# Kernel optimization log

Measured on AMD Instinct MI355X. Metric: run time of the kernel, lower is better.

## Reference

```python
import jax, jax.numpy as jnp
import numpy as np

B, S, DEC, ENC = 64, 4096, 512, 256


def setup_inputs() -> dict:
    key = jax.random.key(0)
    ks = jax.random.split(key, 8)
    scale_d = 1.0 / np.sqrt(DEC)
    scale_e = 1.0 / np.sqrt(ENC)
    return {
        "decoder_hidden": jax.random.normal(ks[0], (B, 1, DEC), jnp.float32),
        "encoder_outputs": jax.random.normal(ks[1], (B, S, ENC), jnp.float32),
        "mask": jax.random.randint(ks[2], (B, S), 0, 2, jnp.int32),
        "Wd": jax.random.normal(ks[3], (DEC, ENC), jnp.float32) * scale_d,
        "bd": jnp.zeros((ENC,), jnp.float32),
        "We": jax.random.normal(ks[4], (ENC, ENC), jnp.float32) * scale_e,
        "be": jnp.zeros((ENC,), jnp.float32),
        "Wa": jax.random.normal(ks[5], (ENC,), jnp.float32) * scale_e,
        "ba": jnp.zeros((1,), jnp.float32),
    }


def reference(decoder_hidden, encoder_outputs, mask, Wd, bd, We, be, Wa, ba):
    # decoder_proj: [B,1,ENC]; encoder_proj: [B,S,ENC]
    decoder_proj = jnp.einsum("bqd,de->bqe", decoder_hidden, Wd) + bd
    encoder_proj = jnp.einsum("bse,ef->bsf", encoder_outputs, We) + be
    energy = jnp.tanh(decoder_proj + encoder_proj)          # [B,S,ENC]
    scores = jnp.einsum("bse,e->bs", energy, Wa) + ba[0]     # [B,S]
    scores = jnp.where(mask == 0, jnp.float32(-1e10), scores)
    attn = jax.nn.softmax(scores, axis=1)                    # [B,S]
    context = jnp.einsum("bs,bse->be", attn, encoder_outputs)[:, None, :]  # [B,1,ENC]
    return context, attn
```

## Files before the change

kernel.cpp:

```cpp
#include <hip/hip_runtime.h>

#define BATCH 64
#define SEQ   4096
#define DECD  512
#define ENC   256
#define TS    128
#define NCHUNK (SEQ / TS)
#define OUT_ATTN (BATCH * ENC)

typedef short  short8  __attribute__((ext_vector_type(8)));
typedef float  floatx4 __attribute__((ext_vector_type(4)));

__device__ __forceinline__ short f2bf(float f) {
    union { float f; unsigned u; } v; v.f = f;
    unsigned u = v.u;
    u += 0x7FFFu + ((u >> 16) & 1u);
    return (short)(u >> 16);
}

__device__ __forceinline__ float fast_tanh(float x) {
    x = fminf(fmaxf(x, -9.0f), 9.0f);
    float e2 = __expf(2.0f * x);
    float r  = __builtin_amdgcn_rcpf(e2 + 1.0f);
    return fmaf(-2.0f, r, 1.0f);
}

__device__ __forceinline__ void gload_lds16(const short* g, short* l) {
    __builtin_amdgcn_global_load_lds(
        (const __attribute__((address_space(1))) unsigned int*)g,
        (__attribute__((address_space(3))) unsigned int*)l,
        16, 0, 0);
}

__global__ void dp_kernel(const float* __restrict__ dh,
                          const float* __restrict__ Wd,
                          const float* __restrict__ bd,
                          const float* __restrict__ be,
                          float* __restrict__ dpb4) {
    __shared__ float dhs[128];
    int blk = blockIdx.x, b = blk >> 2, j = blk & 3;
    int t = threadIdx.x;
    if (t < 128) dhs[t] = dh[b * DECD + j * 128 + t];
    __syncthreads();
    const float* wp = Wd + (size_t)(j * 128) * ENC + t;
    float a0 = 0.f, a1 = 0.f, a2 = 0.f, a3 = 0.f;
#pragma unroll 4
    for (int d = 0; d < 128; d += 4) {
        a0 = fmaf(dhs[d],     wp[(size_t)(d)     * ENC], a0);
        a1 = fmaf(dhs[d + 1], wp[(size_t)(d + 1) * ENC], a1);
        a2 = fmaf(dhs[d + 2], wp[(size_t)(d + 2) * ENC], a2);
        a3 = fmaf(dhs[d + 3], wp[(size_t)(d + 3) * ENC], a3);
    }
    float r = (a0 + a1) + (a2 + a3);
    if (j == 0) r += bd[t] + be[t];
    dpb4[(size_t)(b * 4 + j) * ENC + t] = r;
}

__global__ void pack_kernel(const float* __restrict__ We, short* __restrict__ WeF) {
    int gid  = blockIdx.x * 256 + threadIdx.x;
    int lane = gid & 63;
    int nt   = (gid >> 6) & 15;
    int kt   = gid >> 10;
    int quad = lane >> 4, l16 = lane & 15;
    int n = nt * 16 + l16;
    short8 v;
#pragma unroll
    for (int j = 0; j < 8; ++j) {
        int k = kt * 32 + quad * 8 + j;
        v[j] = f2bf(We[k * ENC + n]);
    }
    *(short8*)(WeF + gid * 8) = v;
}

__global__ __launch_bounds__(512, 4) void main_kernel(
    const float* __restrict__ enc, const int* __restrict__ mask,
    const short* __restrict__ WeF, const float* __restrict__ dpb4,
    const float* __restrict__ Wa, const float* __restrict__ ba,
    float* __restrict__ out, float* __restrict__ ctx_ws, float* __restrict__ ml_ws)
{
    __shared__ short Bs[32768];
    float* F    = (float*)Bs;
    float* scF  = F;
    float* wgtF = F + 128;
    float* dpbF = F + 256;
    float* waF  = F + 512;

    int blk   = blockIdx.x;
    int b     = blk >> 5;
    int chunk = blk & 31;
    int s_base = chunk * TS;
    int t    = threadIdx.x;
    int w    = t >> 6, lane = t & 63;
    int quad = lane >> 4, l16 = lane & 15;

    const float* encB = enc + (size_t)b * SEQ * ENC;
    int row = s_base + w * 16 + l16;
    const float* aRow = encB + (size_t)row * ENC + quad * 8;

    floatx4 acc[16];
#pragma unroll
    for (int nt = 0; nt < 16; ++nt) acc[nt] = (floatx4){0.f, 0.f, 0.f, 0.f};

    floatx4 p0[3], p1[3];
#pragma unroll
    for (int p = 0; p < 3; ++p) {
        p0[p] = *(const floatx4*)(aRow + p * 32);
        p1[p] = *(const floatx4*)(aRow + p * 32 + 4);
    }

#pragma unroll
    for (int j = 0; j < 8; ++j) {
        int c = j * 8 + w;
        gload_lds16(WeF + c * 512 + lane * 8, Bs + c * 512 + lane * 8);
    }
    __syncthreads();

#pragma unroll
    for (int kkt = 0; kkt < 4; ++kkt) {
        const int s = kkt % 3;
        short8 a;
#pragma unroll
        for (int j = 0; j < 4; ++j) { a[j] = f2bf(p0[s][j]); a[j + 4] = f2bf(p1[s][j]); }
        if (kkt < 5) {
            p0[s] = *(const floatx4*)(aRow + (kkt + 3) * 32);
            p1[s] = *(const floatx4*)(aRow + (kkt + 3) * 32 + 4);
        }
        const short* bp = Bs + kkt * 8192 + lane * 8;
#pragma unroll
        for (int ng = 0; ng < 4; ++ng) {
            short8 bf0 = *(const short8*)(bp + (ng * 4 + 0) * 512);
            short8 bf1 = *(const short8*)(bp + (ng * 4 + 1) * 512);
            short8 bf2 = *(const short8*)(bp + (ng * 4 + 2) * 512);
            short8 bf3 = *(const short8*)(bp + (ng * 4 + 3) * 512);
            acc[ng * 4 + 0] = __builtin_amdgcn_mfma_f32_16x16x32_bf16(a, bf0, acc[ng * 4 + 0], 0, 0, 0);
            acc[ng * 4 + 1] = __builtin_amdgcn_mfma_f32_16x16x32_bf16(a, bf1, acc[ng * 4 + 1], 0, 0, 0);
            acc[ng * 4 + 2] = __builtin_amdgcn_mfma_f32_16x16x32_bf16(a, bf2, acc[ng * 4 + 2], 0, 0, 0);
            acc[ng * 4 + 3] = __builtin_amdgcn_mfma_f32_16x16x32_bf16(a, bf3, acc[ng * 4 + 3], 0, 0, 0);
        }
    }

    __syncthreads();
#pragma unroll
    for (int j = 0; j < 8; ++j) {
        int c = j * 8 + w;
        gload_lds16(WeF + 32768 + c * 512 + lane * 8, Bs + c * 512 + lane * 8);
    }
    __syncthreads();

#pragma unroll
    for (int kkt = 4; kkt < 8; ++kkt) {
        const int s = kkt % 3;
        short8 a;
#pragma unroll
        for (int j = 0; j < 4; ++j) { a[j] = f2bf(p0[s][j]); a[j + 4] = f2bf(p1[s][j]); }
        if (kkt < 5) {
            p0[s] = *(const floatx4*)(aRow + (kkt + 3) * 32);
            p1[s] = *(const floatx4*)(aRow + (kkt + 3) * 32 + 4);
        }
        const short* bp = Bs + (kkt - 4) * 8192 + lane * 8;
#pragma unroll
        for (int ng = 0; ng < 4; ++ng) {
            short8 bf0 = *(const short8*)(bp + (ng * 4 + 0) * 512);
            short8 bf1 = *(const short8*)(bp + (ng * 4 + 1) * 512);
            short8 bf2 = *(const short8*)(bp + (ng * 4 + 2) * 512);
            short8 bf3 = *(const short8*)(bp + (ng * 4 + 3) * 512);
            acc[ng * 4 + 0] = __builtin_amdgcn_mfma_f32_16x16x32_bf16(a, bf0, acc[ng * 4 + 0], 0, 0, 0);
            acc[ng * 4 + 1] = __builtin_amdgcn_mfma_f32_16x16x32_bf16(a, bf1, acc[ng * 4 + 1], 0, 0, 0);
            acc[ng * 4 + 2] = __builtin_amdgcn_mfma_f32_16x16x32_bf16(a, bf2, acc[ng * 4 + 2], 0, 0, 0);
            acc[ng * 4 + 3] = __builtin_amdgcn_mfma_f32_16x16x32_bf16(a, bf3, acc[ng * 4 + 3], 0, 0, 0);
        }
    }

    __syncthreads();
    if (t < 256) {
        const float* dp = dpb4 + (size_t)b * 4 * ENC;
        dpbF[t] = dp[t] + dp[ENC + t] + dp[2 * ENC + t] + dp[3 * ENC + t];
    } else {
        waF[t - 256] = Wa[t - 256];
    }
    __syncthreads();

    float ba0 = ba[0];
    float part[4] = {0.f, 0.f, 0.f, 0.f};
#pragma unroll
    for (int nt = 0; nt < 16; ++nt) {
        int n = nt * 16 + l16;
        float wa  = waF[n];
        float dpv = dpbF[n];
#pragma unroll
        for (int r = 0; r < 4; ++r)
            part[r] = fmaf(wa, fast_tanh(acc[nt][r] + dpv), part[r]);
    }
#pragma unroll
    for (int r = 0; r < 4; ++r) {
        float v = part[r];
        v += __shfl_xor(v, 1);
        v += __shfl_xor(v, 2);
        v += __shfl_xor(v, 4);
        v += __shfl_xor(v, 8);
        part[r] = v;
    }
    if (l16 == 0) {
        int idx0 = w * 16 + quad * 4;
        int s0 = s_base + idx0;
        const int4 mv = *(const int4*)(mask + b * SEQ + s0);
        int mvals[4] = {mv.x, mv.y, mv.z, mv.w};
#pragma unroll
        for (int r = 0; r < 4; ++r) {
            float scv = part[r] + ba0;
            if (mvals[r] == 0) scv = -1e10f;
            scF[idx0 + r] = scv;
            out[OUT_ATTN + (size_t)b * SEQ + s0 + r] = scv;
        }
    }
    __syncthreads();

    float v0 = scF[lane], v1 = scF[lane + 64];
    float m = fmaxf(v0, v1);
    m = fmaxf(m, __shfl_xor(m, 1));
    m = fmaxf(m, __shfl_xor(m, 2));
    m = fmaxf(m, __shfl_xor(m, 4));
    m = fmaxf(m, __shfl_xor(m, 8));
    m = fmaxf(m, __shfl_xor(m, 16));
    m = fmaxf(m, __shfl_xor(m, 32));
    float e0 = __expf(v0 - m), e1 = __expf(v1 - m);
    float l = e0 + e1;
    l += __shfl_xor(l, 1);
    l += __shfl_xor(l, 2);
    l += __shfl_xor(l, 4);
    l += __shfl_xor(l, 8);
    l += __shfl_xor(l, 16);
    l += __shfl_xor(l, 32);
    if (t < TS) wgtF[t] = __expf(scF[t] - m);
    __syncthreads();

    int ecol = t & 255, seg = t >> 8;
    float c0 = 0.f, c1 = 0.f, c2 = 0.f, c3 = 0.f;
    const float* ep = encB + (size_t)(s_base + seg * 64) * ENC + ecol;
    const float* wp = wgtF + seg * 64;
#pragma unroll 4
    for (int s2 = 0; s2 < 64; s2 += 4) {
        c0 = fmaf(wp[s2],     ep[(size_t)(s2)     * ENC], c0);
        c1 = fmaf(wp[s2 + 1], ep[(size_t)(s2 + 1) * ENC], c1);
        c2 = fmaf(wp[s2 + 2], ep[(size_t)(s2 + 2) * ENC], c2);
        c3 = fmaf(wp[s2 + 3], ep[(size_t)(s2 + 3) * ENC], c3);
    }
    float ctx = (c0 + c1) + (c2 + c3);

    int cidx = b * NCHUNK + chunk;
    ctx_ws[((size_t)cidx * 2 + seg) * ENC + ecol] = ctx;
    if (t == 0) {
        ml_ws[cidx * 2]     = m;
        ml_ws[cidx * 2 + 1] = l;
    }
}

__global__ void final_kernel(const float* __restrict__ ctx_ws,
                             const float* __restrict__ ml_ws,
                             float* __restrict__ out) {
    int b = blockIdx.x, t = threadIdx.x;
    float m = -3.4e38f;
    for (int c = 0; c < NCHUNK; ++c)
        m = fmaxf(m, ml_ws[(b * NCHUNK + c) * 2]);
    float L = 0.f;
    for (int c = 0; c < NCHUNK; ++c)
        L += ml_ws[(b * NCHUNK + c) * 2 + 1] * __expf(ml_ws[(b * NCHUNK + c) * 2] - m);
    float inv = 1.0f / L;

    float cx = 0.f;
    for (int c = 0; c < NCHUNK; ++c) {
        float sc_c = __expf(ml_ws[(b * NCHUNK + c) * 2] - m);
        size_t base = ((size_t)(b * NCHUNK + c) * 2) * ENC + t;
        cx += sc_c * (ctx_ws[base] + ctx_ws[base + ENC]);
    }
    out[b * ENC + t] = cx * inv;

    for (int s = t; s < SEQ; s += 256) {
        float raw = out[OUT_ATTN + (size_t)b * SEQ + s];
        out[OUT_ATTN + (size_t)b * SEQ + s] = __expf(raw - m) * inv;
    }
}

extern "C" void kernel_launch(void* const* d_in, const int* in_sizes, int n_in,
                              void* d_out, int out_size, void* d_ws, size_t ws_size,
                              hipStream_t stream) {
    const float* dh   = (const float*)d_in[0];
    const float* enc  = (const float*)d_in[1];
    const int*   mask = (const int*)d_in[2];
    const float* Wd   = (const float*)d_in[3];
    const float* bd   = (const float*)d_in[4];
    const float* We   = (const float*)d_in[5];
    const float* be   = (const float*)d_in[6];
    const float* Wa   = (const float*)d_in[7];
    const float* ba   = (const float*)d_in[8];
    float* out = (float*)d_out;

    float* w      = (float*)d_ws;
    float* ctx_ws = w;
    float* ml_ws  = w + BATCH * NCHUNK * 2 * ENC;
    float* dpb4   = ml_ws + BATCH * NCHUNK * 2;
    short* WeF    = (short*)(dpb4 + BATCH * 4 * ENC);

    hipLaunchKernelGGL(dp_kernel,   dim3(BATCH * 4),       dim3(256), 0, stream, dh, Wd, bd, be, dpb4);
    hipLaunchKernelGGL(pack_kernel, dim3(32),              dim3(256), 0, stream, We, WeF);
    hipLaunchKernelGGL(main_kernel, dim3(BATCH * NCHUNK),  dim3(512), 0, stream,
                       enc, mask, WeF, dpb4, Wa, ba, out, ctx_ws, ml_ws);
    hipLaunchKernelGGL(final_kernel, dim3(BATCH),          dim3(256), 0, stream, ctx_ws, ml_ws, out);
}
```

Measured before the change: 416.5 us.

## Reuse register-held bf16 encoder tiles for context, merge prep kernels, widen final grid

The main kernel now loads and converts the whole encoder row slice to bf16 registers up front. The context sum reuses those register values through shuffle reductions and LDS instead of re-reading the encoder tile from global memory. The dp and pack kernels are merged into one launch, and the final kernel is spread over 8 blocks per batch so the attention normalisation runs with more parallelism. In exchange, the context is now computed from bf16-rounded encoder values, which costs precision, and more registers are held live, which may lower occupancy.

After: 491.7 us. +18.1%, slower.

```diff
diff --git a/kernel.cpp b/kernel.cpp
--- a/kernel.cpp
+++ b/kernel.cpp
@@ -18,6 +18,12 @@
     return (short)(u >> 16);
 }
 
+__device__ __forceinline__ float bf2f(short s) {
+    union { unsigned u; float f; } v;
+    v.u = ((unsigned)(unsigned short)s) << 16;
+    return v.f;
+}
+
 __device__ __forceinline__ float fast_tanh(float x) {
     x = fminf(fmaxf(x, -9.0f), 9.0f);
     float e2 = __expf(2.0f * x);
@@ -32,44 +38,47 @@
         16, 0, 0);
 }
 
-__global__ void dp_kernel(const float* __restrict__ dh,
-                          const float* __restrict__ Wd,
-                          const float* __restrict__ bd,
-                          const float* __restrict__ be,
-                          float* __restrict__ dpb4) {
+__global__ void prep_kernel(const float* __restrict__ dh,
+                            const float* __restrict__ Wd,
+                            const float* __restrict__ bd,
+                            const float* __restrict__ be,
+                            const float* __restrict__ We,
+                            float* __restrict__ dpb4,
+                            short* __restrict__ WeF) {
     __shared__ float dhs[128];
-    int blk = blockIdx.x, b = blk >> 2, j = blk & 3;
+    int blk = blockIdx.x;
     int t = threadIdx.x;
-    if (t < 128) dhs[t] = dh[b * DECD + j * 128 + t];
-    __syncthreads();
-    const float* wp = Wd + (size_t)(j * 128) * ENC + t;
-    float a0 = 0.f, a1 = 0.f, a2 = 0.f, a3 = 0.f;
+    if (blk < 256) {
+        int b = blk >> 2, j = blk & 3;
+        if (t < 128) dhs[t] = dh[b * DECD + j * 128 + t];
+        __syncthreads();
+        const float* wp = Wd + (size_t)(j * 128) * ENC + t;
+        float a0 = 0.f, a1 = 0.f, a2 = 0.f, a3 = 0.f;
 #pragma unroll 4
-    for (int d = 0; d < 128; d += 4) {
-        a0 = fmaf(dhs[d],     wp[(size_t)(d)     * ENC], a0);
-        a1 = fmaf(dhs[d + 1], wp[(size_t)(d + 1) * ENC], a1);
-        a2 = fmaf(dhs[d + 2], wp[(size_t)(d + 2) * ENC], a2);
-        a3 = fmaf(dhs[d + 3], wp[(size_t)(d + 3) * ENC], a3);
-    }
-    float r = (a0 + a1) + (a2 + a3);
-    if (j == 0) r += bd[t] + be[t];
-    dpb4[(size_t)(b * 4 + j) * ENC + t] = r;
-}
-
-__global__ void pack_kernel(const float* __restrict__ We, short* __restrict__ WeF) {
-    int gid  = blockIdx.x * 256 + threadIdx.x;
-    int lane = gid & 63;
-    int nt   = (gid >> 6) & 15;
-    int kt   = gid >> 10;
-    int quad = lane >> 4, l16 = lane & 15;
-    int n = nt * 16 + l16;
-    short8 v;
-#pragma unroll
-    for (int j = 0; j < 8; ++j) {
-        int k = kt * 32 + quad * 8 + j;
-        v[j] = f2bf(We[k * ENC + n]);
-    }
-    *(short8*)(WeF + gid * 8) = v;
+        for (int d = 0; d < 128; d += 4) {
+            a0 = fmaf(dhs[d],     wp[(size_t)(d)     * ENC], a0);
+            a1 = fmaf(dhs[d + 1], wp[(size_t)(d + 1) * ENC], a1);
+            a2 = fmaf(dhs[d + 2], wp[(size_t)(d + 2) * ENC], a2);
+            a3 = fmaf(dhs[d + 3], wp[(size_t)(d + 3) * ENC], a3);
+        }
+        float r = (a0 + a1) + (a2 + a3);
+        if (j == 0) r += bd[t] + be[t];
+        dpb4[(size_t)(b * 4 + j) * ENC + t] = r;
+    } else {
+        int gid  = (blk - 256) * 256 + t;
+        int lane = gid & 63;
+        int nt   = (gid >> 6) & 15;
+        int kt   = gid >> 10;
+        int quad = lane >> 4, l16 = lane & 15;
+        int n = nt * 16 + l16;
+        short8 v;
+#pragma unroll
+        for (int j = 0; j < 8; ++j) {
+            int k = kt * 32 + quad * 8 + j;
+            v[j] = f2bf(We[k * ENC + n]);
+        }
+        *(short8*)(WeF + gid * 8) = v;
+    }
 }
 
 __global__ __launch_bounds__(512, 4) void main_kernel(
@@ -84,6 +93,7 @@
     float* wgtF = F + 128;
     float* dpbF = F + 256;
     float* waF  = F + 512;
+    float* ctxF = F + 768;
 
     int blk   = blockIdx.x;
     int b     = blk >> 5;
@@ -97,15 +107,15 @@
     int row = s_base + w * 16 + l16;
     const float* aRow = encB + (size_t)row * ENC + quad * 8;
 
-    floatx4 acc[16];
-#pragma unroll
-    for (int nt = 0; nt < 16; ++nt) acc[nt] = (floatx4){0.f, 0.f, 0.f, 0.f};
-
-    floatx4 p0[3], p1[3];
-#pragma unroll
-    for (int p = 0; p < 3; ++p) {
-        p0[p] = *(const floatx4*)(aRow + p * 32);
-        p1[p] = *(const floatx4*)(aRow + p * 32 + 4);
+    short8 af[8];
+#pragma unroll
+    for (int kkt = 0; kkt < 4; ++kkt) {
+        floatx4 q0 = *(const floatx4*)(aRow + kkt * 32);
+        floatx4 q1 = *(const floatx4*)(aRow + kkt * 32 + 4);
+        short8 a;
+#pragma unroll
+        for (int j = 0; j < 4; ++j) { a[j] = f2bf(q0[j]); a[j + 4] = f2bf(q1[j]); }
+        af[kkt] = a;
     }
 
 #pragma unroll
@@ -113,18 +123,25 @@
         int c = j * 8 + w;
         gload_lds16(WeF + c * 512 + lane * 8, Bs + c * 512 + lane * 8);
     }
+
+#pragma unroll
+    for (int kkt = 4; kkt < 8; ++kkt) {
+        floatx4 q0 = *(const floatx4*)(aRow + kkt * 32);
+        floatx4 q1 = *(const floatx4*)(aRow + kkt * 32 + 4);
+        short8 a;
+#pragma unroll
+        for (int j = 0; j < 4; ++j) { a[j] = f2bf(q0[j]); a[j + 4] = f2bf(q1[j]); }
+        af[kkt] = a;
+    }
+
+    floatx4 acc[16];
+#pragma unroll
+    for (int nt = 0; nt < 16; ++nt) acc[nt] = (floatx4){0.f, 0.f, 0.f, 0.f};
+
     __syncthreads();
 
 #pragma unroll
     for (int kkt = 0; kkt < 4; ++kkt) {
-        const int s = kkt % 3;
-        short8 a;
-#pragma unroll
-        for (int j = 0; j < 4; ++j) { a[j] = f2bf(p0[s][j]); a[j + 4] = f2bf(p1[s][j]); }
-        if (kkt < 5) {
-            p0[s] = *(const floatx4*)(aRow + (kkt + 3) * 32);
-            p1[s] = *(const floatx4*)(aRow + (kkt + 3) * 32 + 4);
-        }
         const short* bp = Bs + kkt * 8192 + lane * 8;
 #pragma unroll
         for (int ng = 0; ng < 4; ++ng) {
@@ -132,10 +149,10 @@
             short8 bf1 = *(const short8*)(bp + (ng * 4 + 1) * 512);
             short8 bf2 = *(const short8*)(bp + (ng * 4 + 2) * 512);
             short8 bf3 = *(const short8*)(bp + (ng * 4 + 3) * 512);
-            acc[ng * 4 + 0] = __builtin_amdgcn_mfma_f32_16x16x32_bf16(a, bf0, acc[ng * 4 + 0], 0, 0, 0);
-            acc[ng * 4 + 1] = __builtin_amdgcn_mfma_f32_16x16x32_bf16(a, bf1, acc[ng * 4 + 1], 0, 0, 0);
-            acc[ng * 4 + 2] = __builtin_amdgcn_mfma_f32_16x16x32_bf16(a, bf2, acc[ng * 4 + 2], 0, 0, 0);
-            acc[ng * 4 + 3] = __builtin_amdgcn_mfma_f32_16x16x32_bf16(a, bf3, acc[ng * 4 + 3], 0, 0, 0);
+            acc[ng * 4 + 0] = __builtin_amdgcn_mfma_f32_16x16x32_bf16(af[kkt], bf0, acc[ng * 4 + 0], 0, 0, 0);
+            acc[ng * 4 + 1] = __builtin_amdgcn_mfma_f32_16x16x32_bf16(af[kkt], bf1, acc[ng * 4 + 1], 0, 0, 0);
+            acc[ng * 4 + 2] = __builtin_amdgcn_mfma_f32_16x16x32_bf16(af[kkt], bf2, acc[ng * 4 + 2], 0, 0, 0);
+            acc[ng * 4 + 3] = __builtin_amdgcn_mfma_f32_16x16x32_bf16(af[kkt], bf3, acc[ng * 4 + 3], 0, 0, 0);
         }
     }
 
@@ -149,14 +166,6 @@
 
 #pragma unroll
     for (int kkt = 4; kkt < 8; ++kkt) {
-        const int s = kkt % 3;
-        short8 a;
-#pragma unroll
-        for (int j = 0; j < 4; ++j) { a[j] = f2bf(p0[s][j]); a[j + 4] = f2bf(p1[s][j]); }
-        if (kkt < 5) {
-            p0[s] = *(const floatx4*)(aRow + (kkt + 3) * 32);
-            p1[s] = *(const floatx4*)(aRow + (kkt + 3) * 32 + 4);
-        }
         const short* bp = Bs + (kkt - 4) * 8192 + lane * 8;
 #pragma unroll
         for (int ng = 0; ng < 4; ++ng) {
@@ -164,10 +173,10 @@
             short8 bf1 = *(const short8*)(bp + (ng * 4 + 1) * 512);
             short8 bf2 = *(const short8*)(bp + (ng * 4 + 2) * 512);
             short8 bf3 = *(const short8*)(bp + (ng * 4 + 3) * 512);
-            acc[ng * 4 + 0] = __builtin_amdgcn_mfma_f32_16x16x32_bf16(a, bf0, acc[ng * 4 + 0], 0, 0, 0);
-            acc[ng * 4 + 1] = __builtin_amdgcn_mfma_f32_16x16x32_bf16(a, bf1, acc[ng * 4 + 1], 0, 0, 0);
-            acc[ng * 4 + 2] = __builtin_amdgcn_mfma_f32_16x16x32_bf16(a, bf2, acc[ng * 4 + 2], 0, 0, 0);
-            acc[ng * 4 + 3] = __builtin_amdgcn_mfma_f32_16x16x32_bf16(a, bf3, acc[ng * 4 + 3], 0, 0, 0);
+            acc[ng * 4 + 0] = __builtin_amdgcn_mfma_f32_16x16x32_bf16(af[kkt], bf0, acc[ng * 4 + 0], 0, 0, 0);
+            acc[ng * 4 + 1] = __builtin_amdgcn_mfma_f32_16x16x32_bf16(af[kkt], bf1, acc[ng * 4 + 1], 0, 0, 0);
+            acc[ng * 4 + 2] = __builtin_amdgcn_mfma_f32_16x16x32_bf16(af[kkt], bf2, acc[ng * 4 + 2], 0, 0, 0);
+            acc[ng * 4 + 3] = __builtin_amdgcn_mfma_f32_16x16x32_bf16(af[kkt], bf3, acc[ng * 4 + 3], 0, 0, 0);
         }
     }
 
@@ -234,21 +243,36 @@
     if (t < TS) wgtF[t] = __expf(scF[t] - m);
     __syncthreads();
 
-    int ecol = t & 255, seg = t >> 8;
-    float c0 = 0.f, c1 = 0.f, c2 = 0.f, c3 = 0.f;
-    const float* ep = encB + (size_t)(s_base + seg * 64) * ENC + ecol;
-    const float* wp = wgtF + seg * 64;
-#pragma unroll 4
-    for (int s2 = 0; s2 < 64; s2 += 4) {
-        c0 = fmaf(wp[s2],     ep[(size_t)(s2)     * ENC], c0);
-        c1 = fmaf(wp[s2 + 1], ep[(size_t)(s2 + 1) * ENC], c1);
-        c2 = fmaf(wp[s2 + 2], ep[(size_t)(s2 + 2) * ENC], c2);
-        c3 = fmaf(wp[s2 + 3], ep[(size_t)(s2 + 3) * ENC], c3);
-    }
-    float ctx = (c0 + c1) + (c2 + c3);
+    float wrow = wgtF[w * 16 + l16];
+#pragma unroll
+    for (int kkt = 0; kkt < 8; ++kkt) {
+        float c[8];
+#pragma unroll
+        for (int j = 0; j < 8; ++j)
+            c[j] = wrow * bf2f(af[kkt][j]);
+#pragma unroll
+        for (int j = 0; j < 8; ++j) {
+            c[j] += __shfl_xor(c[j], 1);
+            c[j] += __shfl_xor(c[j], 2);
+            c[j] += __shfl_xor(c[j], 4);
+            c[j] += __shfl_xor(c[j], 8);
+        }
+        if (l16 == 0) {
+            floatx4 u0 = {c[0], c[1], c[2], c[3]};
+            floatx4 u1 = {c[4], c[5], c[6], c[7]};
+            *(floatx4*)(ctxF + w * 256 + kkt * 32 + quad * 8)     = u0;
+            *(floatx4*)(ctxF + w * 256 + kkt * 32 + quad * 8 + 4) = u1;
+        }
+    }
+    __syncthreads();
 
     int cidx = b * NCHUNK + chunk;
-    ctx_ws[((size_t)cidx * 2 + seg) * ENC + ecol] = ctx;
+    if (t < 256) {
+        float cx = 0.f;
+#pragma unroll
+        for (int w2 = 0; w2 < 8; ++w2) cx += ctxF[w2 * 256 + t];
+        ctx_ws[(size_t)cidx * ENC + t] = cx;
+    }
     if (t == 0) {
         ml_ws[cidx * 2]     = m;
         ml_ws[cidx * 2 + 1] = l;
@@ -258,7 +282,8 @@
 __global__ void final_kernel(const float* __restrict__ ctx_ws,
                              const float* __restrict__ ml_ws,
                              float* __restrict__ out) {
-    int b = blockIdx.x, t = threadIdx.x;
+    int blk = blockIdx.x, b = blk >> 3, j = blk & 7;
+    int t = threadIdx.x;
     float m = -3.4e38f;
     for (int c = 0; c < NCHUNK; ++c)
         m = fmaxf(m, ml_ws[(b * NCHUNK + c) * 2]);
@@ -267,18 +292,20 @@
         L += ml_ws[(b * NCHUNK + c) * 2 + 1] * __expf(ml_ws[(b * NCHUNK + c) * 2] - m);
     float inv = 1.0f / L;
 
-    float cx = 0.f;
-    for (int c = 0; c < NCHUNK; ++c) {
-        float sc_c = __expf(ml_ws[(b * NCHUNK + c) * 2] - m);
-        size_t base = ((size_t)(b * NCHUNK + c) * 2) * ENC + t;
-        cx += sc_c * (ctx_ws[base] + ctx_ws[base + ENC]);
-    }
-    out[b * ENC + t] = cx * inv;
-
-    for (int s = t; s < SEQ; s += 256) {
-        float raw = out[OUT_ATTN + (size_t)b * SEQ + s];
-        out[OUT_ATTN + (size_t)b * SEQ + s] = __expf(raw - m) * inv;
-    }
+    if (j == 0) {
+        float cx = 0.f;
+        for (int c = 0; c < NCHUNK; ++c) {
+            float sc_c = __expf(ml_ws[(b * NCHUNK + c) * 2] - m);
+            cx += sc_c * ctx_ws[(size_t)(b * NCHUNK + c) * ENC + t];
+        }
+        out[b * ENC + t] = cx * inv;
+    }
+
+    size_t base = OUT_ATTN + (size_t)b * SEQ + j * 512;
+    float r0 = out[base + t];
+    float r1 = out[base + 256 + t];
+    out[base + t]       = __expf(r0 - m) * inv;
+    out[base + 256 + t] = __expf(r1 - m) * inv;
 }
 
 extern "C" void kernel_launch(void* const* d_in, const int* in_sizes, int n_in,
@@ -297,13 +324,14 @@
 
     float* w      = (float*)d_ws;
     float* ctx_ws = w;
-    float* ml_ws  = w + BATCH * NCHUNK * 2 * ENC;
+    float* ml_ws  = w + BATCH * NCHUNK * ENC;
     float* dpb4   = ml_ws + BATCH * NCHUNK * 2;
     short* WeF    = (short*)(dpb4 + BATCH * 4 * ENC);
 
-    hipLaunchKernelGGL(dp_kernel,   dim3(BATCH * 4),       dim3(256), 0, stream, dh, Wd, bd, be, dpb4);
-    hipLaunchKernelGGL(pack_kernel, dim3(32),              dim3(256), 0, stream, We, WeF);
-    hipLaunchKernelGGL(main_kernel, dim3(BATCH * NCHUNK),  dim3(512), 0, stream,
+    hipLaunchKernelGGL(prep_kernel,  dim3(256 + 32),       dim3(256), 0, stream,
+                       dh, Wd, bd, be, We, dpb4, WeF);
+    hipLaunchKernelGGL(main_kernel,  dim3(BATCH * NCHUNK), dim3(512), 0, stream,
                        enc, mask, WeF, dpb4, Wa, ba, out, ctx_ws, ml_ws);
-    hipLaunchKernelGGL(final_kernel, dim3(BATCH),          dim3(256), 0, stream, ctx_ws, ml_ws, out);
-}
+    hipLaunchKernelGGL(final_kernel, dim3(BATCH * 8),      dim3(256), 0, stream,
+                       ctx_ws, ml_ws, out);
+}
```
